# Performance work log

Hardware: AMD Instinct MI355X
Metric: run time of the kernel (lower is better)

The kernel has to match this reference:

```python
import jax, jax.numpy as jnp
import numpy as np

EMBED_DIM = 1024
NUM_HEADS = 16
HEAD_DIM = EMBED_DIM // NUM_HEADS


def setup_inputs() -> dict:
    key = jax.random.key(0)
    ks = jax.random.split(key, 6)
    B, S, D = 2, 2048, EMBED_DIM
    scale = 1.0 / np.sqrt(D)
    return {
        "inputs": jax.random.normal(ks[0], (B, S, D), dtype=jnp.float32),
        "Wq": jax.random.normal(ks[1], (D, D), dtype=jnp.float32) * scale,
        "Wk": jax.random.normal(ks[2], (D, D), dtype=jnp.float32) * scale,
        "Wv": jax.random.normal(ks[3], (D, D), dtype=jnp.float32) * scale,
        "Wo": jax.random.normal(ks[4], (D, D), dtype=jnp.float32) * scale,
        "bo": jnp.zeros((D,), dtype=jnp.float32),
    }


def reference(inputs, Wq, Wk, Wv, Wo, bo):
    B, S, D = inputs.shape
    H, P = NUM_HEADS, HEAD_DIM
    # torch Linear: x @ W.T ; weights stored [out, in]
    q = inputs @ Wq.T
    k = inputs @ Wk.T
    v = inputs @ Wv.T
    # separate heads: [B, S, H, P] -> [B, H, S, P]
    q = q.reshape(B, S, H, P).transpose(0, 2, 1, 3)
    k = k.reshape(B, S, H, P).transpose(0, 2, 1, 3)
    v = v.reshape(B, S, H, P).transpose(0, 2, 1, 3)
    # scaled dot-product attention; scale = 1/sqrt(P + 1e-9)
    scale = 1.0 / jnp.sqrt(jnp.float32(P) + 1e-9)
    scores = jnp.einsum("bhsp,bhtp->bhst", q, k) * scale
    weights = jax.nn.softmax(scores, axis=-1)
    attn = jnp.einsum("bhst,bhtp->bhsp", weights, v)
    # merge heads -> [B, S, D]
    concat = attn.transpose(0, 2, 1, 3).reshape(B, S, D)
    return concat @ Wo.T + bo
```

## Files before the change

### kernel.cpp

```cpp
#include <hip/hip_runtime.h>
#include <hip/hip_bf16.h>

typedef __bf16 bf16;
typedef __bf16 bf16x8 __attribute__((ext_vector_type(8)));
typedef float  f32x4  __attribute__((ext_vector_type(4)));

#define QSCALE 0.18033688011112042f

__device__ __forceinline__ void load16_lds(const bf16* g, bf16* l) {
    __builtin_amdgcn_global_load_lds(
        (const __attribute__((address_space(1))) unsigned int*)g,
        (__attribute__((address_space(3))) unsigned int*)l, 16, 0, 0);
}

__global__ void cvt_f32_bf16(
    const float* __restrict__ s0, const float* __restrict__ s1,
    const float* __restrict__ s2, const float* __restrict__ s3,
    const float* __restrict__ s4,
    bf16* __restrict__ d0, bf16* __restrict__ d1, bf16* __restrict__ d2,
    bf16* __restrict__ d3, bf16* __restrict__ d4)
{
    const float* s; bf16* d; int nblk;
    switch (blockIdx.y) {
        case 0:  s = s0; d = d0; nblk = 2048; break;
        case 1:  s = s1; d = d1; nblk = 512;  break;
        case 2:  s = s2; d = d2; nblk = 512;  break;
        case 3:  s = s3; d = d3; nblk = 512;  break;
        default: s = s4; d = d4; nblk = 512;  break;
    }
    if ((int)blockIdx.x >= nblk) return;
    int idx = blockIdx.x * 256 + threadIdx.x;
    float4 a = ((const float4*)s)[idx * 2];
    float4 b = ((const float4*)s)[idx * 2 + 1];
    bf16x8 o;
    o[0] = (bf16)a.x; o[1] = (bf16)a.y; o[2] = (bf16)a.z; o[3] = (bf16)a.w;
    o[4] = (bf16)b.x; o[5] = (bf16)b.y; o[6] = (bf16)b.z; o[7] = (bf16)b.w;
    *(bf16x8*)&d[idx * 8] = o;
}

__global__ __launch_bounds__(256, 2) void qkv_gemm(
    const bf16* __restrict__ A,
    const bf16* __restrict__ Wq, const bf16* __restrict__ Wk,
    const bf16* __restrict__ Wv,
    bf16* __restrict__ qbuf, bf16* __restrict__ kbuf, bf16* __restrict__ vT)
{
    __shared__ bf16 sA[128 * 32];
    __shared__ bf16 sB[128 * 32];

    const int which = blockIdx.x >> 3;
    const int n0    = (blockIdx.x & 7) * 128;
    const int m0    = blockIdx.y * 128;
    const bf16* B   = (which == 0) ? Wq : (which == 1) ? Wk : Wv;

    const int tid  = threadIdx.x;
    const int lane = tid & 63;
    const int w    = tid >> 6;
    const int wr   = w >> 1, wc = w & 1;
    const int r    = lane & 15;
    const int qd   = lane >> 4;

    f32x4 acc[4][4];
    const f32x4 zero4 = {0.f, 0.f, 0.f, 0.f};
#pragma unroll
    for (int mi = 0; mi < 4; ++mi)
#pragma unroll
        for (int ni = 0; ni < 4; ++ni) acc[mi][ni] = zero4;

    for (int kt = 0; kt < 32; ++kt) {
        const bf16* gA = A + (size_t)m0 * 1024 + kt * 32;
        const bf16* gB = B + (size_t)n0 * 1024 + kt * 32;
        __syncthreads();
#pragma unroll
        for (int j = 0; j < 2; ++j) {
            int task = j * 256 + tid;
            int row  = task >> 2, ch = task & 3;
            int ldsb = (j * 256 + w * 64) * 8;
            load16_lds(gA + (size_t)row * 1024 + ch * 8, &sA[ldsb]);
            load16_lds(gB + (size_t)row * 1024 + ch * 8, &sB[ldsb]);
        }
        __syncthreads();

        bf16x8 af[4], bfr[4];
#pragma unroll
        for (int mi = 0; mi < 4; ++mi)
            af[mi] = *(const bf16x8*)&sA[(wr * 64 + mi * 16 + r) * 32 + qd * 8];
#pragma unroll
        for (int ni = 0; ni < 4; ++ni)
            bfr[ni] = *(const bf16x8*)&sB[(wc * 64 + ni * 16 + r) * 32 + qd * 8];
#pragma unroll
        for (int mi = 0; mi < 4; ++mi)
#pragma unroll
            for (int ni = 0; ni < 4; ++ni)
                acc[mi][ni] = __builtin_amdgcn_mfma_f32_16x16x32_bf16(
                    af[mi], bfr[ni], acc[mi][ni], 0, 0, 0);
    }

    const float scale = (which == 0) ? QSCALE : 1.0f;
#pragma unroll
    for (int mi = 0; mi < 4; ++mi)
#pragma unroll
        for (int ni = 0; ni < 4; ++ni)
#pragma unroll
            for (int i = 0; i < 4; ++i) {
                int row = m0 + wr * 64 + mi * 16 + qd * 4 + i;
                int col = n0 + wc * 64 + ni * 16 + r;
                float v = acc[mi][ni][i] * scale;
                if (which == 0) {
                    qbuf[(size_t)row * 1024 + col] = (bf16)v;
                } else if (which == 1) {
                    kbuf[(size_t)row * 1024 + col] = (bf16)v;
                } else {
                    vT[((size_t)((row >> 11) * 1024 + col)) * 2048 + (row & 2047)] = (bf16)v;
                }
            }
}

__global__ __launch_bounds__(256, 2) void out_gemm(
    const bf16* __restrict__ A, const bf16* __restrict__ B,
    float* __restrict__ C, const float* __restrict__ bias)
{
    __shared__ bf16 sA[128 * 32];
    __shared__ bf16 sB[64 * 32];

    const int tid  = threadIdx.x;
    const int lane = tid & 63;
    const int w    = tid >> 6;
    const int wr   = w >> 1, wc = w & 1;
    const int r    = lane & 15;
    const int qd   = lane >> 4;
    const int m0   = blockIdx.y * 128;
    const int n0   = blockIdx.x * 64;

    f32x4 acc[4][2];
    const f32x4 zero4 = {0.f, 0.f, 0.f, 0.f};
#pragma unroll
    for (int mi = 0; mi < 4; ++mi)
#pragma unroll
        for (int ni = 0; ni < 2; ++ni) acc[mi][ni] = zero4;

    for (int kt = 0; kt < 32; ++kt) {
        const bf16* gA = A + (size_t)m0 * 1024 + kt * 32;
        const bf16* gB = B + (size_t)n0 * 1024 + kt * 32;
        __syncthreads();
#pragma unroll
        for (int j = 0; j < 2; ++j) {
            int task = j * 256 + tid;
            int row  = task >> 2, ch = task & 3;
            int ldsb = (j * 256 + w * 64) * 8;
            load16_lds(gA + (size_t)row * 1024 + ch * 8, &sA[ldsb]);
        }
        {
            int row = tid >> 2, ch = tid & 3;
            int ldsb = (w * 64) * 8;
            load16_lds(gB + (size_t)row * 1024 + ch * 8, &sB[ldsb]);
        }
        __syncthreads();

        bf16x8 af[4], bfr[2];
#pragma unroll
        for (int mi = 0; mi < 4; ++mi)
            af[mi] = *(const bf16x8*)&sA[(wr * 64 + mi * 16 + r) * 32 + qd * 8];
#pragma unroll
        for (int ni = 0; ni < 2; ++ni)
            bfr[ni] = *(const bf16x8*)&sB[(wc * 32 + ni * 16 + r) * 32 + qd * 8];
#pragma unroll
        for (int mi = 0; mi < 4; ++mi)
#pragma unroll
            for (int ni = 0; ni < 2; ++ni)
                acc[mi][ni] = __builtin_amdgcn_mfma_f32_16x16x32_bf16(
                    af[mi], bfr[ni], acc[mi][ni], 0, 0, 0);
    }

#pragma unroll
    for (int mi = 0; mi < 4; ++mi)
#pragma unroll
        for (int ni = 0; ni < 2; ++ni)
#pragma unroll
            for (int i = 0; i < 4; ++i) {
                int row = m0 + wr * 64 + mi * 16 + qd * 4 + i;
                int col = n0 + wc * 32 + ni * 16 + r;
                C[(size_t)row * 1024 + col] = acc[mi][ni][i] + bias[col];
            }
}

__global__ __launch_bounds__(256, 2) void attn_kernel(
    const bf16* __restrict__ qbuf, const bf16* __restrict__ kbuf,
    const bf16* __restrict__ vT, bf16* __restrict__ concat)
{
    __shared__ bf16 sK[64 * 72];
    __shared__ bf16 sV[80 * 72];
    __shared__ bf16 sP[128 * 72];

    const int tid  = threadIdx.x;
    const int lane = tid & 63;
    const int w    = tid >> 6;
    const int r    = lane & 15;
    const int qd   = lane >> 4;
    const int qt   = blockIdx.x;
    const int bh   = blockIdx.y;
    const int b    = bh >> 4, h = bh & 15;
    const int qrow0 = b * 2048 + qt * 128;
    const size_t vbase = (size_t)bh * 64 * 2048;
    const int rk4 = (r >> 2) & 3;

    for (int e = tid; e < 16 * 72; e += 256) {
        int rr = e / 72, cc = e % 72;
        sV[(64 + rr) * 72 + cc] = (rr == 0 && cc < 64) ? (bf16)1.0f : (bf16)0.0f;
    }

    bf16x8 aq[2][2];
#pragma unroll
    for (int mi = 0; mi < 2; ++mi)
#pragma unroll
        for (int ks = 0; ks < 2; ++ks)
            aq[mi][ks] = *(const bf16x8*)&qbuf[
                (size_t)(qrow0 + w * 32 + mi * 16 + r) * 1024 + h * 64 + ks * 32 + qd * 8];

    f32x4 acc_o[2][4], acc_l[2];
    const f32x4 zero4 = {0.f, 0.f, 0.f, 0.f};
#pragma unroll
    for (int mi = 0; mi < 2; ++mi) {
        acc_l[mi] = zero4;
#pragma unroll
        for (int nj = 0; nj < 4; ++nj) acc_o[mi][nj] = zero4;
    }

    for (int tt = 0; tt < 32; ++tt) {
        bf16x8 rk[2], rv[2];
        int krow[2], kch[2];
#pragma unroll
        for (int t = 0; t < 2; ++t) {
            int flat = t * 256 + tid;
            krow[t] = flat >> 3; kch[t] = flat & 7;
            rk[t] = *(const bf16x8*)&kbuf[(size_t)(b * 2048 + tt * 64 + krow[t]) * 1024 + h * 64 + kch[t] * 8];
            rv[t] = *(const bf16x8*)&vT[vbase + (size_t)krow[t] * 2048 + tt * 64 + kch[t] * 8];
        }
        __syncthreads();
#pragma unroll
        for (int t = 0; t < 2; ++t) {
            *(bf16x8*)&sK[krow[t] * 72 + kch[t] * 8] = rk[t];
            *(bf16x8*)&sV[krow[t] * 72 + kch[t] * 8] = rv[t];
        }
        __syncthreads();

        f32x4 accs[2][4];
#pragma unroll
        for (int mi = 0; mi < 2; ++mi)
#pragma unroll
            for (int ni = 0; ni < 4; ++ni) accs[mi][ni] = zero4;
#pragma unroll
        for (int ks = 0; ks < 2; ++ks)
#pragma unroll
            for (int ni = 0; ni < 4; ++ni) {
                bf16x8 bk = *(const bf16x8*)&sK[(ni * 16 + r) * 72 + ks * 32 + qd * 8];
#pragma unroll
                for (int mi = 0; mi < 2; ++mi)
                    accs[mi][ni] = __builtin_amdgcn_mfma_f32_16x16x32_bf16(
                        aq[mi][ks], bk, accs[mi][ni], 0, 0, 0);
            }

#pragma unroll
        for (int mi = 0; mi < 2; ++mi)
#pragma unroll
            for (int i = 0; i < 4; ++i) {
                int prow = w * 32 + mi * 16 + qd * 4 + i;
#pragma unroll
                for (int ni = 0; ni < 4; ++ni)
                    sP[prow * 72 + ((ni * 16 + r) ^ (qd * 16))] =
                        (bf16)exp2f(accs[mi][ni][i]);
            }

#pragma unroll
        for (int ks = 0; ks < 2; ++ks) {
            bf16x8 ap[2];
#pragma unroll
            for (int mi = 0; mi < 2; ++mi)
                ap[mi] = *(const bf16x8*)&sP[(w * 32 + mi * 16 + r) * 72 +
                                             (((ks * 32 + qd * 8) ^ (rk4 * 16)))];
#pragma unroll
            for (int nj = 0; nj < 4; ++nj) {
                bf16x8 bv = *(const bf16x8*)&sV[(nj * 16 + r) * 72 + ks * 32 + qd * 8];
#pragma unroll
                for (int mi = 0; mi < 2; ++mi)
                    acc_o[mi][nj] = __builtin_amdgcn_mfma_f32_16x16x32_bf16(
                        ap[mi], bv, acc_o[mi][nj], 0, 0, 0);
            }
            {
                bf16x8 bv1 = *(const bf16x8*)&sV[(64 + r) * 72 + ks * 32 + qd * 8];
#pragma unroll
                for (int mi = 0; mi < 2; ++mi)
                    acc_l[mi] = __builtin_amdgcn_mfma_f32_16x16x32_bf16(
                        ap[mi], bv1, acc_l[mi], 0, 0, 0);
            }
        }
    }

#pragma unroll
    for (int mi = 0; mi < 2; ++mi)
#pragma unroll
        for (int i = 0; i < 4; ++i) {
            float l   = __shfl(acc_l[mi][i], lane & 48);
            float inv = 1.0f / l;
            int grow  = qrow0 + w * 32 + mi * 16 + qd * 4 + i;
#pragma unroll
            for (int nj = 0; nj < 4; ++nj) {
                int gcol = h * 64 + nj * 16 + r;
                concat[(size_t)grow * 1024 + gcol] = (bf16)(acc_o[mi][nj][i] * inv);
            }
        }
}

extern "C" void kernel_launch(void* const* d_in, const int* in_sizes, int n_in,
                              void* d_out, int out_size, void* d_ws, size_t ws_size,
                              hipStream_t stream)
{
    const float* x  = (const float*)d_in[0];
    const float* Wq = (const float*)d_in[1];
    const float* Wk = (const float*)d_in[2];
    const float* Wv = (const float*)d_in[3];
    const float* Wo = (const float*)d_in[4];
    const float* bo = (const float*)d_in[5];
    float* out = (float*)d_out;

    char* ws = (char*)d_ws;
    bf16* xb     = (bf16*)(ws);
    bf16* Wqb    = (bf16*)(ws + (8u  << 20));
    bf16* Wkb    = (bf16*)(ws + (10u << 20));
    bf16* Wvb    = (bf16*)(ws + (12u << 20));
    bf16* Wob    = (bf16*)(ws + (14u << 20));
    bf16* qbuf   = (bf16*)(ws + (16u << 20));
    bf16* kbuf   = (bf16*)(ws + (24u << 20));
    bf16* vT     = (bf16*)(ws + (32u << 20));
    bf16* concat = (bf16*)(ws + (40u << 20));

    hipLaunchKernelGGL(cvt_f32_bf16, dim3(2048, 5), dim3(256), 0, stream,
                       x, Wq, Wk, Wv, Wo, xb, Wqb, Wkb, Wvb, Wob);
    hipLaunchKernelGGL(qkv_gemm, dim3(24, 32), dim3(256), 0, stream,
                       xb, Wqb, Wkb, Wvb, qbuf, kbuf, vT);
    hipLaunchKernelGGL(attn_kernel, dim3(16, 32), dim3(256), 0, stream,
                       qbuf, kbuf, vT, concat);
    hipLaunchKernelGGL(out_gemm, dim3(16, 32), dim3(256), 0, stream,
                       concat, Wob, out, bo);
}
```

Measured before the change: 213.9 us.

## Keep softmax probabilities in registers via transposed S MFMA, drop P shared buffer

Computes the score tile transposed (K as the A operand) so each lane's exp2 results form the B operand of 16x16x16 bf16 MFMAs for the PV product. This removes the sP shared-memory round trip and its extra LDS traffic. The row-sum now uses a ones vector instead of an extra V row in shared memory. Output is staged through shared memory for coalesced 16-byte stores. The PV step uses the older 16x16x16 instruction, so it issues more MFMAs per tile.

New measurement: 215.8 us. About the same (+0.8%).

```diff
diff --git a/kernel.cpp b/kernel.cpp
--- a/kernel.cpp
+++ b/kernel.cpp
@@ -2,7 +2,9 @@
 #include <hip/hip_bf16.h>
 
 typedef __bf16 bf16;
+typedef __bf16 bf16x4 __attribute__((ext_vector_type(4)));
 typedef __bf16 bf16x8 __attribute__((ext_vector_type(8)));
+typedef short  s16x4  __attribute__((ext_vector_type(4)));
 typedef float  f32x4  __attribute__((ext_vector_type(4)));
 
 #define QSCALE 0.18033688011112042f
@@ -187,9 +189,9 @@
     const bf16* __restrict__ qbuf, const bf16* __restrict__ kbuf,
     const bf16* __restrict__ vT, bf16* __restrict__ concat)
 {
-    __shared__ bf16 sK[64 * 72];
-    __shared__ bf16 sV[80 * 72];
-    __shared__ bf16 sP[128 * 72];
+    __shared__ bf16 smem[2 * 64 * 72];
+    bf16* sK = smem;
+    bf16* sV = smem + 64 * 72;
 
     const int tid  = threadIdx.x;
     const int lane = tid & 63;
@@ -201,12 +203,8 @@
     const int b    = bh >> 4, h = bh & 15;
     const int qrow0 = b * 2048 + qt * 128;
     const size_t vbase = (size_t)bh * 64 * 2048;
-    const int rk4 = (r >> 2) & 3;
-
-    for (int e = tid; e < 16 * 72; e += 256) {
-        int rr = e / 72, cc = e % 72;
-        sV[(64 + rr) * 72 + cc] = (rr == 0 && cc < 64) ? (bf16)1.0f : (bf16)0.0f;
-    }
+
+    const s16x4 ones4 = {(short)0x3F80, (short)0x3F80, (short)0x3F80, (short)0x3F80};
 
     bf16x8 aq[2][2];
 #pragma unroll
@@ -222,7 +220,7 @@
     for (int mi = 0; mi < 2; ++mi) {
         acc_l[mi] = zero4;
 #pragma unroll
-        for (int nj = 0; nj < 4; ++nj) acc_o[mi][nj] = zero4;
+        for (int pj = 0; pj < 4; ++pj) acc_o[mi][pj] = zero4;
     }
 
     for (int tt = 0; tt < 32; ++tt) {
@@ -252,62 +250,65 @@
         for (int ks = 0; ks < 2; ++ks)
 #pragma unroll
             for (int ni = 0; ni < 4; ++ni) {
-                bf16x8 bk = *(const bf16x8*)&sK[(ni * 16 + r) * 72 + ks * 32 + qd * 8];
+                bf16x8 ak = *(const bf16x8*)&sK[(ni * 16 + r) * 72 + ks * 32 + qd * 8];
 #pragma unroll
                 for (int mi = 0; mi < 2; ++mi)
                     accs[mi][ni] = __builtin_amdgcn_mfma_f32_16x16x32_bf16(
-                        aq[mi][ks], bk, accs[mi][ni], 0, 0, 0);
-            }
-
+                        ak, aq[mi][ks], accs[mi][ni], 0, 0, 0);
+            }
+
+        s16x4 pfrag[2][4];
 #pragma unroll
         for (int mi = 0; mi < 2; ++mi)
 #pragma unroll
-            for (int i = 0; i < 4; ++i) {
-                int prow = w * 32 + mi * 16 + qd * 4 + i;
-#pragma unroll
-                for (int ni = 0; ni < 4; ++ni)
-                    sP[prow * 72 + ((ni * 16 + r) ^ (qd * 16))] =
-                        (bf16)exp2f(accs[mi][ni][i]);
-            }
-
-#pragma unroll
-        for (int ks = 0; ks < 2; ++ks) {
-            bf16x8 ap[2];
+            for (int ni = 0; ni < 4; ++ni) {
+                bf16x4 pv;
+#pragma unroll
+                for (int i = 0; i < 4; ++i) pv[i] = (bf16)exp2f(accs[mi][ni][i]);
+                pfrag[mi][ni] = __builtin_bit_cast(s16x4, pv);
+            }
+
+#pragma unroll
+        for (int ni = 0; ni < 4; ++ni) {
+#pragma unroll
+            for (int pj = 0; pj < 4; ++pj) {
+                bf16x4 av = *(const bf16x4*)&sV[(pj * 16 + r) * 72 + ni * 16 + qd * 4];
+                s16x4  avs = __builtin_bit_cast(s16x4, av);
+#pragma unroll
+                for (int mi = 0; mi < 2; ++mi)
+                    acc_o[mi][pj] = __builtin_amdgcn_mfma_f32_16x16x16bf16_1k(
+                        avs, pfrag[mi][ni], acc_o[mi][pj], 0, 0, 0);
+            }
 #pragma unroll
             for (int mi = 0; mi < 2; ++mi)
-                ap[mi] = *(const bf16x8*)&sP[(w * 32 + mi * 16 + r) * 72 +
-                                             (((ks * 32 + qd * 8) ^ (rk4 * 16)))];
-#pragma unroll
-            for (int nj = 0; nj < 4; ++nj) {
-                bf16x8 bv = *(const bf16x8*)&sV[(nj * 16 + r) * 72 + ks * 32 + qd * 8];
-#pragma unroll
-                for (int mi = 0; mi < 2; ++mi)
-                    acc_o[mi][nj] = __builtin_amdgcn_mfma_f32_16x16x32_bf16(
-                        ap[mi], bv, acc_o[mi][nj], 0, 0, 0);
-            }
-            {
-                bf16x8 bv1 = *(const bf16x8*)&sV[(64 + r) * 72 + ks * 32 + qd * 8];
-#pragma unroll
-                for (int mi = 0; mi < 2; ++mi)
-                    acc_l[mi] = __builtin_amdgcn_mfma_f32_16x16x32_bf16(
-                        ap[mi], bv1, acc_l[mi], 0, 0, 0);
-            }
-        }
-    }
-
-#pragma unroll
-    for (int mi = 0; mi < 2; ++mi)
-#pragma unroll
-        for (int i = 0; i < 4; ++i) {
-            float l   = __shfl(acc_l[mi][i], lane & 48);
-            float inv = 1.0f / l;
-            int grow  = qrow0 + w * 32 + mi * 16 + qd * 4 + i;
-#pragma unroll
-            for (int nj = 0; nj < 4; ++nj) {
-                int gcol = h * 64 + nj * 16 + r;
-                concat[(size_t)grow * 1024 + gcol] = (bf16)(acc_o[mi][nj][i] * inv);
-            }
-        }
+                acc_l[mi] = __builtin_amdgcn_mfma_f32_16x16x16bf16_1k(
+                    ones4, pfrag[mi][ni], acc_l[mi], 0, 0, 0);
+        }
+    }
+
+    __syncthreads();
+    bf16* scratch = smem;
+#pragma unroll
+    for (int mi = 0; mi < 2; ++mi) {
+        float inv = 1.0f / acc_l[mi][0];
+        int qloc  = w * 32 + mi * 16 + r;
+#pragma unroll
+        for (int pj = 0; pj < 4; ++pj)
+#pragma unroll
+            for (int i = 0; i < 4; ++i)
+                scratch[qloc * 64 + pj * 16 + qd * 4 + i] =
+                    (bf16)(acc_o[mi][pj][i] * inv);
+    }
+    __syncthreads();
+    {
+        int row  = tid >> 1;
+        int half = tid & 1;
+#pragma unroll
+        for (int c = 0; c < 4; ++c) {
+            bf16x8 v = *(const bf16x8*)&scratch[row * 64 + half * 32 + c * 8];
+            *(bf16x8*)&concat[(size_t)(qrow0 + row) * 1024 + h * 64 + half * 32 + c * 8] = v;
+        }
+    }
 }
 
 extern "C" void kernel_launch(void* const* d_in, const int* in_sizes, int n_in,
```
